# Performance work log

Measured on AMD Instinct MI355X. Metric: run time of the kernel, lower is better.

The kernel has to match this reference:

```python
import jax, jax.numpy as jnp
import numpy as np
from jax import lax

HMA = 8.0
H = W = 34
A = 15
IMH = IMW = 270.0
AW = jnp.array([9.232984,16.0,27.712813,18.465969,32.0,55.425626,36.931937,64.0,110.851252,73.863875,128.0,221.702503,147.72775,256.0,443.405007], jnp.float32)
AH = jnp.array([27.72668,16.0,9.237604,55.453359,32.0,18.475209,110.906719,64.0,36.950417,221.813438,128.0,73.900834,443.626876,256.0,147.801669], jnp.float32)
RPN_MEAN = jnp.array([0.000437,0.002586,-0.123953,-0.081469], jnp.float32)
RPN_STD = jnp.array([0.12677,0.095741,0.3173,0.281042], jnp.float32)
RCNN_STD = jnp.array([0.1,0.1,0.2,0.2], jnp.float32)
RPN_MIN = 6.16056
RCNN_MIN = 8.8008
NUM_CLASS = 3

def _decode(t, acx, acy, aw, ah):
    cx = t[..., 0] * aw + acx
    cy = t[..., 1] * ah + acy
    bw = jnp.exp(t[..., 2]) * aw
    bh = jnp.exp(t[..., 3]) * ah
    x1 = jnp.clip(cx - 0.5 * (bw - 1.0), 0.0, IMW - 1.0)
    y1 = jnp.clip(cy - 0.5 * (bh - 1.0), 0.0, IMH - 1.0)
    x2 = jnp.clip(cx + 0.5 * (bw - 1.0), 0.0, IMW - 1.0)
    y2 = jnp.clip(cy + 0.5 * (bh - 1.0), 0.0, IMH - 1.0)
    return jnp.stack([x1, y1, x2, y2], -1)

def _nms(boxes, scores, thresh, top_n):
    # greedy hard NMS, fixed top_n output with validity mask
    x1, y1, x2, y2 = boxes[:, 0], boxes[:, 1], boxes[:, 2], boxes[:, 3]
    areas = (x2 - x1 + 1.0) * (y2 - y1 + 1.0)
    n = boxes.shape[0]
    def step(scur, _):
        j = jnp.argmax(scur)
        valid = scur[j] > 0.0
        bj = boxes[j]
        iw = jnp.maximum(jnp.minimum(x2, bj[2]) - jnp.maximum(x1, bj[0]) + 1.0, 0.0)
        ih = jnp.maximum(jnp.minimum(y2, bj[3]) - jnp.maximum(y1, bj[1]) + 1.0, 0.0)
        inter = iw * ih
        iou = inter / (areas + areas[j] - inter)
        sup = (iou > thresh) | (jnp.arange(n) == j)
        return jnp.where(sup, -1.0, scur), (j, valid)
    _, (idx, valid) = lax.scan(step, scores, None, length=top_n)
    return idx, valid

def _psroi_one(ftr, roi):
    # ftr: [10,7,7,H,W] position-sensitive features; roi: [x1,y1,x2,y2] image coords
    sw = roi[0] / HMA; sh = roi[1] / HMA
    ew = (roi[2] + 1.0) / HMA; eh = (roi[3] + 1.0) / HMA
    rh = jnp.maximum(eh - sh, 0.1); rw = jnp.maximum(ew - sw, 0.1)
    bh = rh / 7.0; bw = rw / 7.0
    g = jnp.arange(7, dtype=jnp.float32); s = jnp.arange(4, dtype=jnp.float32)
    ys = sh + g[:, None] * bh + (s[None, :] + 0.5) * (bh / 4.0)  # [7(ph),4]
    xs = sw + g[:, None] * bw + (s[None, :] + 0.5) * (bw / 4.0)  # [7(pw),4]
    y0 = jnp.floor(ys); x0 = jnp.floor(xs)
    dy = ys - y0; dx = xs - x0
    y0i = y0.astype(jnp.int32); x0i = x0.astype(jnp.int32)
    c = jnp.arange(10)[:, None, None, None, None]
    P = jnp.arange(7)[None, :, None, None, None]
    Q = jnp.arange(7)[None, None, :, None, None]
    def corner(yi, xi, wy, wx):
        my = ((yi >= 0) & (yi < H)).astype(jnp.float32)
        mx = ((xi >= 0) & (xi < W)).astype(jnp.float32)
        yc = jnp.clip(yi, 0, H - 1); xc = jnp.clip(xi, 0, W - 1)
        v = ftr[c, P, Q, yc[None, :, None, :, None], xc[None, None, :, None, :]]
        return v * (wy * my)[None, :, None, :, None] * (wx * mx)[None, None, :, None, :]
    val = (corner(y0i, x0i, 1 - dy, 1 - dx) + corner(y0i, x0i + 1, 1 - dy, dx)
         + corner(y0i + 1, x0i, dy, 1 - dx) + corner(y0i + 1, x0i + 1, dy, dx))
    return val.mean(axis=(3, 4))  # [10,7,7]

def reference(rpn_cls_prob_reshape, rpn_bbox_pred, ft_add_left_right, W_inner, b_inner, W_cls, b_cls, W_bbox, b_bbox):
    # ---------- RPNProposalSSD ----------
    fg = rpn_cls_prob_reshape[0, A:, :, :].reshape(-1)  # [A*H*W] fg probs
    t = rpn_bbox_pred[0].reshape(A, 4, H, W).transpose(0, 2, 3, 1)  # [A,H,W,4]
    t = t * RPN_STD + RPN_MEAN
    acx = (jnp.arange(W, dtype=jnp.float32) * HMA)[None, None, :]
    acy = (jnp.arange(H, dtype=jnp.float32) * HMA)[None, :, None]
    boxes = _decode(t, acx, acy, AW[:, None, None], AH[:, None, None]).reshape(-1, 4)
    bw = boxes[:, 2] - boxes[:, 0] + 1.0; bh = boxes[:, 3] - boxes[:, 1] + 1.0
    keep = (fg >= 0.2) & ((bw >= RPN_MIN) | (bh >= RPN_MIN))
    top_s, top_i = lax.top_k(jnp.where(keep, fg, -1.0), 3000)
    cand = boxes[top_i]
    idx, valid = _nms(cand, top_s, 0.7, 300)
    vm = valid.astype(jnp.float32)[:, None]
    rois_xy = cand[idx] * vm  # [300,4], padded rows zeroed
    rois = jnp.concatenate([jnp.zeros((300, 1), jnp.float32), rois_xy], axis=1)
    rpn_scores = top_s[idx][:, None] * vm  # [300,1]
    # ---------- DFMBPSROIAlign ----------
    ftr = ft_add_left_right[0].reshape(10, 7, 7, H, W)
    pooled = jax.vmap(lambda r: _psroi_one(ftr, r))(rois_xy)  # [300,10,7,7]
    # ---------- FC head ----------
    feat = jax.nn.relu(pooled.reshape(-1, 490) @ W_inner.T + b_inner)
    probs = jax.nn.softmax(feat @ W_cls.T + b_cls, axis=1)  # [300,4]
    bpred = feat @ W_bbox.T + b_bbox  # [300,16]
    # ---------- RCNNProposal ----------
    rw = rois_xy[:, 2] - rois_xy[:, 0] + 1.0; rh2 = rois_xy[:, 3] - rois_xy[:, 1] + 1.0
    rcx = rois_xy[:, 0] + 0.5 * (rw - 1.0); rcy = rois_xy[:, 1] + 0.5 * (rh2 - 1.0)
    obj_ok = (1.0 - probs[:, 0]) >= 0.1
    all_b, all_s, all_l, all_k = [], [], [], []
    for cidx in range(1, NUM_CLASS + 1):
        tc = bpred[:, 4 * cidx:4 * cidx + 4] * RCNN_STD  # rcnn mean is 0
        db = _decode(tc, rcx, rcy, rw, rh2)
        dw = db[:, 2] - db[:, 0] + 1.0; dh = db[:, 3] - db[:, 1] + 1.0
        sc = probs[:, cidx]
        k = valid & obj_ok & (sc >= 0.1) & ((dw >= RCNN_MIN) | (dh >= RCNN_MIN))
        all_b.append(db); all_s.append(sc)
        all_l.append(jnp.full((300,), float(cidx), jnp.float32)); all_k.append(k)
    cb = jnp.concatenate(all_b); cs = jnp.concatenate(all_s)
    cl = jnp.concatenate(all_l); ck = jnp.concatenate(all_k)
    ts2, ti2 = lax.top_k(jnp.where(ck, cs, -1.0), 300)
    cand2 = cb[ti2]; lab2 = cl[ti2]
    idx2, val2 = _nms(cand2, ts2, 0.5, 5)
    v2 = val2.astype(jnp.float32)
    bboxes = jnp.concatenate([cand2[idx2] * v2[:, None], (ts2[idx2] * v2)[:, None], (lab2[idx2] * v2)[:, None]], axis=1)  # [5,6] x1,y1,x2,y2,score,label
    return bboxes, rois, rpn_scores

def setup_inputs() -> dict:
    key = jax.random.key(0)
    ks = jax.random.split(key, 6)
    return {
        'rpn_cls_prob_reshape': jax.random.uniform(ks[0], (1, 2 * A, H, W), jnp.float32),
        'rpn_bbox_pred': jax.random.normal(ks[1], (1, 4 * A, H, W), jnp.float32) * 0.5,
        'ft_add_left_right': jax.random.normal(ks[2], (1, 490, H, W), jnp.float32),
        'W_inner': jax.random.normal(ks[3], (2048, 490), jnp.float32) * 0.02,
        'b_inner': jnp.zeros((2048,), jnp.float32),
        'W_cls': jax.random.normal(ks[4], (4, 2048), jnp.float32) * 0.02,
        'b_cls': jnp.zeros((4,), jnp.float32),
        'W_bbox': jax.random.normal(ks[5], (16, 2048), jnp.float32) * 0.02,
        'b_bbox': jnp.zeros((16,), jnp.float32),
    }
```

## Files before the change

kernel.cpp:

```cpp
#include <hip/hip_runtime.h>

#define NB 17340
#define TOPK1 3000
#define TOPK2 300
#define PTS 304

__constant__ float c_AW[15] = {9.232984, 16.0, 27.712813, 18.465969, 32.0, 55.425626,
                               36.931937, 64.0, 110.851252, 73.863875, 128.0, 221.702503,
                               147.72775, 256.0, 443.405007};
__constant__ float c_AH[15] = {27.72668, 16.0, 9.237604, 55.453359, 32.0, 18.475209,
                               110.906719, 64.0, 36.950417, 221.813438, 128.0, 73.900834,
                               443.626876, 256.0, 147.801669};

__device__ __forceinline__ unsigned mapf(float f) {
  unsigned u = __float_as_uint(f);
  return (u & 0x80000000u) ? ~u : (u | 0x80000000u);
}
__device__ __forceinline__ float unmapf(unsigned m) {
  unsigned u = (m & 0x80000000u) ? (m & 0x7FFFFFFFu) : ~m;
  return __uint_as_float(u);
}
__device__ __forceinline__ float clipc(float v) {
  return fminf(fmaxf(v, 0.0f), 269.0f);
}
__device__ __forceinline__ unsigned long long readlane64(unsigned long long v, int lane) {
  unsigned lo = (unsigned)__builtin_amdgcn_readlane((int)(unsigned)v, lane);
  unsigned hi = (unsigned)__builtin_amdgcn_readlane((int)(unsigned)(v >> 32), lane);
  return ((unsigned long long)hi << 32) | lo;
}

__global__ void k_decode(const float* __restrict__ cls, const float* __restrict__ pred,
                         float* __restrict__ boxes, float* __restrict__ scores,
                         unsigned int* __restrict__ hist) {
  int i = blockIdx.x * 256 + threadIdx.x;
  if (i >= NB) return;
  int a = i / 1156;
  int rem = i - a * 1156;
  int y = rem / 34;
  int x = rem - y * 34;
  float fg = cls[(15 + a) * 1156 + rem];
  const float* p = pred + a * 4 * 1156 + rem;
  float t0 = p[0]    * (float)0.12677  + (float)0.000437;
  float t1 = p[1156] * (float)0.095741 + (float)0.002586;
  float t2 = p[2312] * (float)0.3173   + (float)-0.123953;
  float t3 = p[3468] * (float)0.281042 + (float)-0.081469;
  float aw = c_AW[a], ah = c_AH[a];
  float cx = t0 * aw + (float)x * 8.0f;
  float cy = t1 * ah + (float)y * 8.0f;
  float bw = expf(t2) * aw;
  float bh = expf(t3) * ah;
  float x1 = clipc(cx - 0.5f * (bw - 1.0f));
  float y1 = clipc(cy - 0.5f * (bh - 1.0f));
  float x2 = clipc(cx + 0.5f * (bw - 1.0f));
  float y2 = clipc(cy + 0.5f * (bh - 1.0f));
  boxes[i * 4 + 0] = x1;
  boxes[i * 4 + 1] = y1;
  boxes[i * 4 + 2] = x2;
  boxes[i * 4 + 3] = y2;
  float w2 = x2 - x1 + 1.0f, h2 = y2 - y1 + 1.0f;
  bool keep = (fg >= 0.2f) && ((w2 >= (float)6.16056) || (h2 >= (float)6.16056));
  scores[i] = keep ? fg : -1.0f;
  if (keep) atomicAdd(&hist[mapf(fg) >> 18], 1u);
}

__global__ __launch_bounds__(256) void k_cutoff(const unsigned int* __restrict__ hist,
                                                unsigned int* __restrict__ bcut) {
  const int t = threadIdx.x;
  __shared__ unsigned int sh[16384];
  __shared__ unsigned int coarse[256];
  for (int i = t; i < 16384; i += 256) sh[i] = hist[i];
  __syncthreads();
  {
    unsigned s = 0;
    int b0 = t * 64;
    for (int b = 0; b < 64; ++b) s += sh[b0 + b];
    coarse[t] = s;
  }
  __syncthreads();
  if (t == 0) {
    unsigned acc = 0, nbefore = 0;
    int C = 0;
    for (int c = 255; c >= 0; --c) {
      if (acc + coarse[c] >= (unsigned)TOPK1) { C = c; nbefore = acc; break; }
      acc += coarse[c];
    }
    unsigned acc2 = nbefore;
    int B = C * 64;
    for (int b = C * 64 + 63; b >= C * 64; --b) {
      if (acc2 + sh[b] >= (unsigned)TOPK1) { B = b; break; }
      acc2 += sh[b];
    }
    bcut[0] = (unsigned)B;
  }
}

__global__ __launch_bounds__(256) void k_compact(const float* __restrict__ scores,
                                                 const unsigned int* __restrict__ bcut,
                                                 unsigned int* __restrict__ cnt,
                                                 unsigned long long* __restrict__ keys) {
  int i = blockIdx.x * 256 + threadIdx.x;
  const unsigned B = bcut[0];
  if (i < NB) {
    unsigned m = mapf(scores[i]);
    if ((m >> 18) >= B) {
      unsigned p = atomicAdd(cnt, 1u);
      if (p < 4096u) keys[p] = ((unsigned long long)m << 15) | (unsigned)(32767 - i);
    }
  }
}

__global__ __launch_bounds__(256) void k_sort(const float* __restrict__ boxes,
                                              const unsigned int* __restrict__ cnt,
                                              const unsigned long long* __restrict__ keys,
                                              unsigned int* __restrict__ sscore,
                                              float4* __restrict__ sbox) {
  const int t = threadIdx.x;
  __shared__ unsigned long long lk[4096];
  const int K = min((int)cnt[0], 4096);
  for (int i = t; i < 4096; i += 256) lk[i] = (i < K) ? keys[i] : 0ull;
  __syncthreads();
  int p = blockIdx.x * 32 + (t >> 3);
  const int s = t & 7;
  if (p < K) {
    unsigned long long kp = lk[p];
    int r = 0;
    for (int q = s; q < 4096; q += 64) {
#pragma unroll
      for (int u = 0; u < 8; ++u) r += (lk[q + 8 * u] > kp) ? 1 : 0;
    }
    r += __shfl_xor(r, 1);
    r += __shfl_xor(r, 2);
    r += __shfl_xor(r, 4);
    if (s == 0 && r < TOPK1) {
      int idx = 32767 - (int)(kp & 32767ull);
      sscore[r] = (unsigned)(kp >> 15);
      sbox[r] = ((const float4*)boxes)[idx];
    }
  }
}

__global__ __launch_bounds__(64) void k_iou(const float4* __restrict__ sbox,
                                            unsigned long long* __restrict__ mat) {
  const int wi = blockIdx.x, wj = blockIdx.y;
  if (wj < wi) return;
  __shared__ float4 cb[64];
  __shared__ float car[64];
  const int l = threadIdx.x;
  float4 c = sbox[wj * 64 + l];
  cb[l] = c;
  car[l] = (c.z - c.x + 1.0f) * (c.w - c.y + 1.0f);
  __syncthreads();
  const int ri = wi * 64 + l;
  float4 r = sbox[ri];
  float rar = (r.z - r.x + 1.0f) * (r.w - r.y + 1.0f);
  unsigned long long m = 0ull;
#pragma unroll 16
  for (int j = 0; j < 64; ++j) {
    float4 cc = cb[j];
    float iw = fmaxf(fminf(r.z, cc.z) - fmaxf(r.x, cc.x) + 1.0f, 0.0f);
    float ih = fmaxf(fminf(r.w, cc.w) - fmaxf(r.y, cc.y) + 1.0f, 0.0f);
    float inter = iw * ih;
    float iou = inter / (car[j] + rar - inter);
    if (iou > 0.7f) m |= (1ull << j);
  }
  mat[ri * 48 + wj] = m;
}

__global__ __launch_bounds__(256) void k_nms1(const unsigned int* __restrict__ sscore,
                                              const float4* __restrict__ sbox,
                                              const unsigned long long* __restrict__ mat,
                                              float* __restrict__ dout,
                                              float* __restrict__ rois_xy,
                                              float* __restrict__ validf) {
  const int t = threadIdx.x;
  __shared__ unsigned long long rowbuf[2][64][48];
  __shared__ unsigned int sc[3008];
  __shared__ int arank[300];
  __shared__ int s_A;
  for (int i = t; i < 3008; i += 256) sc[i] = (i < TOPK1) ? sscore[i] : 0u;
  if (t == 0) s_A = 0;

  {
    unsigned long long r0v[12];
#pragma unroll
    for (int i = 0; i < 12; ++i) r0v[i] = mat[t + 256 * i];
#pragma unroll
    for (int i = 0; i < 12; ++i) {
      int idx = t + 256 * i;
      rowbuf[0][idx / 48][idx % 48] = r0v[i];
    }
  }
  unsigned long long rgA[16], rgB[16];
  const int st = t - 64;
  if (t >= 64) {
#pragma unroll
    for (int i = 0; i < 16; ++i) rgA[i] = mat[1 * 3072 + st + 192 * i];
#pragma unroll
    for (int i = 0; i < 16; ++i) rgB[i] = mat[2 * 3072 + st + 192 * i];
  }
  __syncthreads();

  unsigned long long run = 0ull;
  int A = 0;
  const int l = t & 63;
  const int lw = (l < 48) ? l : 0;
  for (int c = 0; c < 47; ++c) {
    if (t < 64) {
      const bool okw = (l >= c) && (l < 47);
      unsigned long long supw = readlane64(run, c);
      bool aliveb = (sc[c * 64 + l] > 0x80000000u) && !((supw >> l) & 1ull);
      unsigned long long alive = __ballot(aliveb);
      int Aw = A;
      const int buf = c & 1;
      while (alive != 0ull && Aw < 300) {
        int j1 = __ffsll((long long)alive) - 1;
        unsigned long long rest = alive & (alive - 1ull);
        int j2 = (rest != 0ull) ? (__ffsll((long long)rest) - 1) : -1;
        unsigned long long v1 = rowbuf[buf][j1][lw];
        unsigned long long v2 = rowbuf[buf][(j2 >= 0 ? j2 : j1)][lw];
        if (l == 0) arank[Aw] = c * 64 + j1;
        Aw++;
        unsigned long long kill1 = readlane64(v1, c);
        run |= okw ? v1 : 0ull;
        alive &= ~kill1;
        if (j2 >= 0 && ((alive >> j2) & 1ull) && Aw < 300) {
          if (l == 0) arank[Aw] = c * 64 + j2;
          Aw++;
          unsigned long long kill2 = readlane64(v2, c);
          run |= okw ? v2 : 0ull;
          alive &= ~kill2;
        }
      }
      A = Aw;
      if (l == 0) s_A = Aw;
    } else if (c < 46) {
      int nb = (c + 1) & 1;
      if (((c + 1) & 1) == 1) {
#pragma unroll
        for (int i = 0; i < 16; ++i) {
          int idx = st + 192 * i;
          rowbuf[nb][idx / 48][idx % 48] = rgA[i];
        }
        if (c + 3 <= 46) {
#pragma unroll
          for (int i = 0; i < 16; ++i) rgA[i] = mat[(c + 3) * 3072 + st + 192 * i];
        }
      } else {
#pragma unroll
        for (int i = 0; i < 16; ++i) {
          int idx = st + 192 * i;
          rowbuf[nb][idx / 48][idx % 48] = rgB[i];
        }
        if (c + 3 <= 46) {
#pragma unroll
          for (int i = 0; i < 16; ++i) rgB[i] = mat[(c + 3) * 3072 + st + 192 * i];
        }
      }
    }
    __syncthreads();
    A = s_A;
    if (A >= 300) break;
    if (c < 46 && sc[(c + 1) * 64] <= 0x80000000u) break;
  }
  for (int a = t; a < A; a += 256) {
    int rk = arank[a];
    float4 b = sbox[rk];
    dout[30 + a * 5 + 0] = 0.0f;
    dout[30 + a * 5 + 1] = b.x;
    dout[30 + a * 5 + 2] = b.y;
    dout[30 + a * 5 + 3] = b.z;
    dout[30 + a * 5 + 4] = b.w;
    dout[1530 + a] = unmapf(sc[rk]);
    rois_xy[a * 4 + 0] = b.x; rois_xy[a * 4 + 1] = b.y;
    rois_xy[a * 4 + 2] = b.z; rois_xy[a * 4 + 3] = b.w;
    validf[a] = 1.0f;
  }
  for (int z = 30 + A * 5 + t; z < 1530; z += 256) dout[z] = 0.f;
  for (int z = 1530 + A + t; z < 1830; z += 256) dout[z] = 0.f;
  for (int z = A * 4 + t; z < 1200; z += 256) rois_xy[z] = 0.f;
  for (int z = A + t; z < 300; z += 256) validf[z] = 0.f;
}

__global__ __launch_bounds__(256) void k_psroi(const float* __restrict__ ft,
                                               const float* __restrict__ rois_xy,
                                               float* __restrict__ pooledT) {
  int r = blockIdx.x;
  __shared__ int2 ycs[28];
  __shared__ float2 wys[28];
  __shared__ int2 xcs[28];
  __shared__ float2 wxs[28];
  float r0 = rois_xy[r * 4 + 0], r1 = rois_xy[r * 4 + 1];
  float r2 = rois_xy[r * 4 + 2], r3 = rois_xy[r * 4 + 3];
  float sw = r0 * 0.125f;
  float sh = r1 * 0.125f;
  float ew = (r2 + 1.0f) * 0.125f;
  float eh = (r3 + 1.0f) * 0.125f;
  float rh = fmaxf(eh - sh, 0.1f);
  float rw = fmaxf(ew - sw, 0.1f);
  float bh = rh / 7.0f;
  float bwd = rw / 7.0f;
  const int t = threadIdx.x;
  if (t < 28) {
    int p = t >> 2, sy = t & 3;
    float ys = sh + (float)p * bh + ((float)sy + 0.5f) * (bh * 0.25f);
    float y0f = floorf(ys);
    float dy = ys - y0f;
    int y0 = (int)y0f;
    float wy0 = (1.0f - dy) * ((y0 >= 0 && y0 < 34) ? 1.f : 0.f);
    float wy1 = dy * ((y0 + 1 >= 0 && y0 + 1 < 34) ? 1.f : 0.f);
    ycs[t] = make_int2(min(max(y0, 0), 33), min(max(y0 + 1, 0), 33));
    wys[t] = make_float2(wy0, wy1);
  } else if (t >= 32 && t < 60) {
    int q = (t - 32) >> 2, sx = (t - 32) & 3;
    float xs = sw + (float)q * bwd + ((float)sx + 0.5f) * (bwd * 0.25f);
    float x0f = floorf(xs);
    float dx = xs - x0f;
    int x0 = (int)x0f;
    float wx0 = (1.0f - dx) * ((x0 >= 0 && x0 < 34) ? 1.f : 0.f);
    float wx1 = dx * ((x0 + 1 >= 0 && x0 + 1 < 34) ? 1.f : 0.f);
    xcs[t - 32] = make_int2(min(max(x0, 0), 33), min(max(x0 + 1, 0), 33));
    wxs[t - 32] = make_float2(wx0, wx1);
  }
  __syncthreads();
  for (int o = t; o < 490; o += 256) {
    int pq = o % 49;
    int p = pq / 7, q = pq - p * 7;
    const float* base = ft + o * 1156;
    float acc = 0.f;
#pragma unroll
    for (int sy = 0; sy < 4; ++sy) {
      int2 yc = ycs[p * 4 + sy];
      float2 wy = wys[p * 4 + sy];
#pragma unroll
      for (int sx = 0; sx < 4; ++sx) {
        int2 xc = xcs[q * 4 + sx];
        float2 wx = wxs[q * 4 + sx];
        float v00 = base[yc.x * 34 + xc.x], v01 = base[yc.x * 34 + xc.y];
        float v10 = base[yc.y * 34 + xc.x], v11 = base[yc.y * 34 + xc.y];
        acc += wy.x * wx.x * v00 + wy.x * wx.y * v01 + wy.y * wx.x * v10 + wy.y * wx.y * v11;
      }
    }
    pooledT[o * PTS + r] = acc * (1.0f / 16.0f);
  }
}

__global__ __launch_bounds__(256) void k_fc1(const float* __restrict__ pooledT,
                                             const float* __restrict__ Wi,
                                             const float* __restrict__ bi,
                                             float* __restrict__ feat) {
  __shared__ float As[2][32][68];
  __shared__ float Bs[2][32][36];
  const int t = threadIdx.x;
  const int tr = t >> 4, tc = t & 15;
  const int b = blockIdx.x;
  const int xcd = b & 7, s = b >> 3;
  const int r0 = (s % 5) * 64;
  const int o0 = (xcd + 8 * (s / 5)) * 32;
  float acc[4][2];
#pragma unroll
  for (int i = 0; i < 4; ++i) { acc[i][0] = 0.f; acc[i][1] = 0.f; }
  float ra[8], rb[4];

#pragma unroll
  for (int i = 0; i < 8; ++i) {
    int idx = t + 256 * i;
    int kk = idx >> 6, rr = idx & 63;
    ra[i] = (kk < 490 && r0 + rr < 300) ? pooledT[kk * PTS + r0 + rr] : 0.f;
  }
#pragma unroll
  for (int i = 0; i < 4; ++i) {
    int idx = t + 256 * i;
    int oo = idx >> 5, k2 = idx & 31;
    rb[i] = Wi[(o0 + oo) * 490 + k2];
  }
#pragma unroll
  for (int i = 0; i < 8; ++i) {
    int idx = t + 256 * i;
    As[0][idx >> 6][idx & 63] = ra[i];
  }
#pragma unroll
  for (int i = 0; i < 4; ++i) {
    int idx = t + 256 * i;
    Bs[0][idx & 31][idx >> 5] = rb[i];
  }
  __syncthreads();

  int cur = 0;
  for (int step = 0; step < 16; ++step) {
    if (step < 15) {
      int k0n = (step + 1) * 32;
#pragma unroll
      for (int i = 0; i < 8; ++i) {
        int idx = t + 256 * i;
        int kk = idx >> 6, rr = idx & 63;
        int k = k0n + kk;
        ra[i] = (k < 490 && r0 + rr < 300) ? pooledT[k * PTS + r0 + rr] : 0.f;
      }
#pragma unroll
      for (int i = 0; i < 4; ++i) {
        int idx = t + 256 * i;
        int oo = idx >> 5, k2 = k0n + (idx & 31);
        rb[i] = (k2 < 490) ? Wi[(o0 + oo) * 490 + k2] : 0.f;
      }
    }
#pragma unroll
    for (int kk = 0; kk < 32; ++kk) {
      float4 a4 = *(const float4*)&As[cur][kk][tr * 4];
      float2 b2 = *(const float2*)&Bs[cur][kk][tc * 2];
      acc[0][0] += a4.x * b2.x; acc[0][1] += a4.x * b2.y;
      acc[1][0] += a4.y * b2.x; acc[1][1] += a4.y * b2.y;
      acc[2][0] += a4.z * b2.x; acc[2][1] += a4.z * b2.y;
      acc[3][0] += a4.w * b2.x; acc[3][1] += a4.w * b2.y;
    }
    if (step < 15) {
      int nxt = cur ^ 1;
#pragma unroll
      for (int i = 0; i < 8; ++i) {
        int idx = t + 256 * i;
        As[nxt][idx >> 6][idx & 63] = ra[i];
      }
#pragma unroll
      for (int i = 0; i < 4; ++i) {
        int idx = t + 256 * i;
        Bs[nxt][idx & 31][idx >> 5] = rb[i];
      }
      cur = nxt;
    }
    __syncthreads();
  }
  float2 bias = *(const float2*)&bi[o0 + tc * 2];
#pragma unroll
  for (int i = 0; i < 4; ++i) {
    int r = r0 + tr * 4 + i;
    if (r < 300) {
      float2 v;
      v.x = fmaxf(acc[i][0] + bias.x, 0.f);
      v.y = fmaxf(acc[i][1] + bias.y, 0.f);
      *(float2*)&feat[r * 2048 + o0 + tc * 2] = v;
    }
  }
}

__global__ __launch_bounds__(256) void k_fc2(const float* __restrict__ feat,
                                             const float* __restrict__ Wc,
                                             const float* __restrict__ bc,
                                             const float* __restrict__ Wb,
                                             const float* __restrict__ bb,
                                             const float* __restrict__ rois_xy,
                                             const float* __restrict__ validf,
                                             float* __restrict__ db2,
                                             float* __restrict__ msc2) {
  int r = blockIdx.x;
  int t = threadIdx.x;
  int l = t & 63, w = t >> 6;
  __shared__ float frow[2048];
  __shared__ float s_logit[20];
  __shared__ float s_probs[4];
  for (int i = t; i < 512; i += 256)
    ((float4*)frow)[i] = ((const float4*)(feat + r * 2048))[i];
  __syncthreads();
  for (int o = w; o < 20; o += 4) {
    const float* wr = (o < 4) ? (Wc + o * 2048) : (Wb + (o - 4) * 2048);
    float p = 0.f;
#pragma unroll
    for (int j = 0; j < 8; ++j) {
      float4 wv = ((const float4*)wr)[l + 64 * j];
      float4 fv = ((const float4*)frow)[l + 64 * j];
      p += wv.x * fv.x + wv.y * fv.y + wv.z * fv.z + wv.w * fv.w;
    }
    for (int off = 32; off > 0; off >>= 1) p += __shfl_xor(p, off);
    if (l == 0) s_logit[o] = p + ((o < 4) ? bc[o] : bb[o - 4]);
  }
  __syncthreads();
  if (t == 0) {
    float m = fmaxf(fmaxf(s_logit[0], s_logit[1]), fmaxf(s_logit[2], s_logit[3]));
    float e0 = expf(s_logit[0] - m), e1 = expf(s_logit[1] - m);
    float e2 = expf(s_logit[2] - m), e3 = expf(s_logit[3] - m);
    float ssum = e0 + e1 + e2 + e3;
    s_probs[0] = e0 / ssum; s_probs[1] = e1 / ssum;
    s_probs[2] = e2 / ssum; s_probs[3] = e3 / ssum;
  }
  __syncthreads();
  if (t < 3) {
    int c = t + 1;
    float x1 = rois_xy[r * 4 + 0], y1 = rois_xy[r * 4 + 1];
    float x2 = rois_xy[r * 4 + 2], y2 = rois_xy[r * 4 + 3];
    float rwv = x2 - x1 + 1.0f, rhv = y2 - y1 + 1.0f;
    float rcx = x1 + 0.5f * (rwv - 1.0f), rcy = y1 + 0.5f * (rhv - 1.0f);
    float t0 = s_logit[4 + 4 * c + 0] * 0.1f;
    float t1 = s_logit[4 + 4 * c + 1] * 0.1f;
    float t2 = s_logit[4 + 4 * c + 2] * 0.2f;
    float t3 = s_logit[4 + 4 * c + 3] * 0.2f;
    float cx = t0 * rwv + rcx, cy = t1 * rhv + rcy;
    float bw = expf(t2) * rwv, bh = expf(t3) * rhv;
    float dx1 = clipc(cx - 0.5f * (bw - 1.0f));
    float dy1 = clipc(cy - 0.5f * (bh - 1.0f));
    float dx2 = clipc(cx + 0.5f * (bw - 1.0f));
    float dy2 = clipc(cy + 0.5f * (bh - 1.0f));
    float dw = dx2 - dx1 + 1.0f, dh = dy2 - dy1 + 1.0f;
    float sc = s_probs[c];
    bool objok = (1.0f - s_probs[0]) >= 0.1f;
    bool valid = validf[r] > 0.5f;
    bool kf = valid && objok && (sc >= 0.1f) && ((dw >= (float)8.8008) || (dh >= (float)8.8008));
    int i2 = (c - 1) * 300 + r;
    db2[i2 * 4 + 0] = dx1; db2[i2 * 4 + 1] = dy1;
    db2[i2 * 4 + 2] = dx2; db2[i2 * 4 + 3] = dy2;
    msc2[i2] = kf ? sc : -1.0f;
  }
}

__global__ __launch_bounds__(1024) void k_nms2(const float* __restrict__ db2,
                                               const float* __restrict__ msc2,
                                               float* __restrict__ dout) {
  const int t = threadIdx.x;
  __shared__ unsigned long long lk[1024];
  __shared__ unsigned long long sk[1024];
  __shared__ float4 abox[5];
  __shared__ float aar[5];
  __shared__ int s_A;
  sk[t] = 0ull;
  lk[t] = (t < 900) ? (((unsigned long long)mapf(msc2[t]) << 10) | (unsigned)(1023 - t)) : 0ull;
  if (t == 0) s_A = 0;
  __syncthreads();
  if (t < 900) {
    unsigned long long kp = lk[t];
    int r = 0;
#pragma unroll 8
    for (int q = 0; q < 1024; ++q) r += (lk[q] > kp) ? 1 : 0;
    sk[r] = kp;
  }
  __syncthreads();
  if (t < 64) {
    int A = 0;
    for (int base = 0; base < TOPK2 && A < 5; base += 64) {
      unsigned headm = (unsigned)(sk[base] >> 10);
      if (headm <= 0x80000000u) break;
      int rank = base + t;
      unsigned long long key = sk[rank];
      unsigned mk = (unsigned)(key >> 10);
      bool active = (rank < TOPK2) && (mk > 0x80000000u);
      int idx = 1023 - (int)(key & 1023ull);
      float4 bx = make_float4(0.f, 0.f, 0.f, 0.f);
      float area = 0.f;
      if (active) {
        bx = ((const float4*)db2)[idx];
        area = (bx.z - bx.x + 1.0f) * (bx.w - bx.y + 1.0f);
      }
      bool alive = active;
      for (int a = 0; a < A; ++a) {
        float4 ab = abox[a];
        float iw = fmaxf(fminf(bx.z, ab.z) - fmaxf(bx.x, ab.x) + 1.0f, 0.0f);
        float ih = fmaxf(fminf(bx.w, ab.w) - fmaxf(bx.y, ab.y) + 1.0f, 0.0f);
        float inter = iw * ih;
        float iou = inter / (area + aar[a] - inter);
        if (iou > 0.5f) { alive = false; break; }
      }
      unsigned long long bal = __ballot(alive);
      while (bal != 0ull && A < 5) {
        int j = __ffsll((long long)bal) - 1;
        float jx1 = __shfl(bx.x, j), jy1 = __shfl(bx.y, j);
        float jx2 = __shfl(bx.z, j), jy2 = __shfl(bx.w, j);
        float jar = __shfl(area, j);
        if (t == j) {
          abox[A] = bx; aar[A] = area;
          dout[A * 6 + 0] = bx.x; dout[A * 6 + 1] = bx.y;
          dout[A * 6 + 2] = bx.z; dout[A * 6 + 3] = bx.w;
          dout[A * 6 + 4] = unmapf(mk);
          dout[A * 6 + 5] = (float)(idx / 300 + 1);
        }
        if (alive) {
          float iw = fmaxf(fminf(bx.z, jx2) - fmaxf(bx.x, jx1) + 1.0f, 0.0f);
          float ih = fmaxf(fminf(bx.w, jy2) - fmaxf(bx.y, jy1) + 1.0f, 0.0f);
          float inter = iw * ih;
          float iou = inter / (area + jar - inter);
          if (iou > 0.5f || t == j) alive = false;
        }
        A++;
        bal = __ballot(alive);
      }
    }
    if (t == 0) s_A = A;
  }
  __syncthreads();
  int A = s_A;
  for (int z = A * 6 + t; z < 30; z += 1024) dout[z] = 0.f;
}

extern "C" void kernel_launch(void* const* d_in, const int* in_sizes, int n_in,
                              void* d_out, int out_size, void* d_ws, size_t ws_size,
                              hipStream_t stream) {
  const float* cls  = (const float*)d_in[0];
  const float* pred = (const float*)d_in[1];
  const float* ft   = (const float*)d_in[2];
  const float* Wi   = (const float*)d_in[3];
  const float* bi   = (const float*)d_in[4];
  const float* Wc   = (const float*)d_in[5];
  const float* bc   = (const float*)d_in[6];
  const float* Wb   = (const float*)d_in[7];
  const float* bb   = (const float*)d_in[8];
  float* out = (float*)d_out;
  float* w = (float*)d_ws;
  float* boxes   = w;
  float* scores  = w + 69360;
  unsigned int* hist = (unsigned int*)(w + 86700);
  unsigned int* cnt  = (unsigned int*)(w + 103084);
  unsigned int* bcut = (unsigned int*)(w + 103085);
  unsigned long long* keys = (unsigned long long*)(w + 103088);
  unsigned int* sscore = (unsigned int*)(w + 111280);
  float4* sbox   = (float4*)(w + 114280);
  float* rois_xy = w + 126312;
  float* validf  = w + 127512;
  float* pooledT = w + 127812;
  float* feat    = w + 276772;
  unsigned long long* mat = (unsigned long long*)(w + 276772);
  float* db2     = w + 891172;
  float* msc2    = w + 894772;

  hipMemsetAsync(hist, 0, 16385 * sizeof(unsigned int), stream);
  k_decode<<<68, 256, 0, stream>>>(cls, pred, boxes, scores, hist);
  k_cutoff<<<1, 256, 0, stream>>>(hist, bcut);
  k_compact<<<68, 256, 0, stream>>>(scores, bcut, cnt, keys);
  k_sort<<<128, 256, 0, stream>>>(boxes, cnt, keys, sscore, sbox);
  k_iou<<<dim3(47, 47), 64, 0, stream>>>(sbox, mat);
  k_nms1<<<1, 256, 0, stream>>>(sscore, sbox, mat, out, rois_xy, validf);
  k_psroi<<<300, 256, 0, stream>>>(ft, rois_xy, pooledT);
  k_fc1<<<320, 256, 0, stream>>>(pooledT, Wi, bi, feat);
  k_fc2<<<300, 256, 0, stream>>>(feat, Wc, bc, Wb, bb, rois_xy, validf, db2, msc2);
  k_nms2<<<1, 1024, 0, stream>>>(db2, msc2, out);
}
```

Baseline: 195.4 us.

## Fuse proposal front-end stages into one cooperative persistent kernel

Merges the histogram memset, decode, cutoff, compaction, rank sort, IoU bitmask and first NMS into one cooperative kernel of 128 blocks. Grid-wide syncs separate the stages, replacing six kernel launches and a memset. The goal is to remove per-launch overhead and inter-kernel gaps across these small stages. In exchange it pays for five grid barriers, and the IoU tiles now run as a grid-stride loop over 4 waves per block instead of one block per tile.

```diff
diff --git a/kernel.cpp b/kernel.cpp
--- a/kernel.cpp
+++ b/kernel.cpp
@@ -1,4 +1,6 @@
 #include <hip/hip_runtime.h>
+#include <hip/hip_cooperative_groups.h>
+namespace cg = cooperative_groups;
 
 #define NB 17340
 #define TOPK1 3000
@@ -29,256 +31,280 @@
   return ((unsigned long long)hi << 32) | lo;
 }
 
-__global__ void k_decode(const float* __restrict__ cls, const float* __restrict__ pred,
-                         float* __restrict__ boxes, float* __restrict__ scores,
-                         unsigned int* __restrict__ hist) {
-  int i = blockIdx.x * 256 + threadIdx.x;
-  if (i >= NB) return;
-  int a = i / 1156;
-  int rem = i - a * 1156;
-  int y = rem / 34;
-  int x = rem - y * 34;
-  float fg = cls[(15 + a) * 1156 + rem];
-  const float* p = pred + a * 4 * 1156 + rem;
-  float t0 = p[0]    * (float)0.12677  + (float)0.000437;
-  float t1 = p[1156] * (float)0.095741 + (float)0.002586;
-  float t2 = p[2312] * (float)0.3173   + (float)-0.123953;
-  float t3 = p[3468] * (float)0.281042 + (float)-0.081469;
-  float aw = c_AW[a], ah = c_AH[a];
-  float cx = t0 * aw + (float)x * 8.0f;
-  float cy = t1 * ah + (float)y * 8.0f;
-  float bw = expf(t2) * aw;
-  float bh = expf(t3) * ah;
-  float x1 = clipc(cx - 0.5f * (bw - 1.0f));
-  float y1 = clipc(cy - 0.5f * (bh - 1.0f));
-  float x2 = clipc(cx + 0.5f * (bw - 1.0f));
-  float y2 = clipc(cy + 0.5f * (bh - 1.0f));
-  boxes[i * 4 + 0] = x1;
-  boxes[i * 4 + 1] = y1;
-  boxes[i * 4 + 2] = x2;
-  boxes[i * 4 + 3] = y2;
-  float w2 = x2 - x1 + 1.0f, h2 = y2 - y1 + 1.0f;
-  bool keep = (fg >= 0.2f) && ((w2 >= (float)6.16056) || (h2 >= (float)6.16056));
-  scores[i] = keep ? fg : -1.0f;
-  if (keep) atomicAdd(&hist[mapf(fg) >> 18], 1u);
-}
-
-__global__ __launch_bounds__(256) void k_cutoff(const unsigned int* __restrict__ hist,
-                                                unsigned int* __restrict__ bcut) {
+__global__ __launch_bounds__(256) void k_front(const float* __restrict__ cls,
+                                               const float* __restrict__ pred,
+                                               float* __restrict__ boxes,
+                                               float* __restrict__ scores,
+                                               unsigned int* __restrict__ hist,
+                                               unsigned int* __restrict__ bcut,
+                                               unsigned int* __restrict__ cnt,
+                                               unsigned long long* __restrict__ keys,
+                                               unsigned int* __restrict__ sscore,
+                                               float4* __restrict__ sbox,
+                                               unsigned long long* __restrict__ mat,
+                                               float* __restrict__ dout,
+                                               float* __restrict__ rois_xy,
+                                               float* __restrict__ validf) {
+  cg::grid_group grid = cg::this_grid();
+  __shared__ __align__(16) unsigned char smem[66560];
   const int t = threadIdx.x;
-  __shared__ unsigned int sh[16384];
-  __shared__ unsigned int coarse[256];
-  for (int i = t; i < 16384; i += 256) sh[i] = hist[i];
-  __syncthreads();
+  const int b = blockIdx.x;
+  const int gid = b * 256 + t;
+  const int gstride = gridDim.x * 256;
+
+  for (int i = gid; i < 16385; i += gstride) hist[i] = 0u;
+  __threadfence();
+  grid.sync();
+
+  for (int i = gid; i < NB; i += gstride) {
+    int a = i / 1156;
+    int rem = i - a * 1156;
+    int y = rem / 34;
+    int x = rem - y * 34;
+    float fg = cls[(15 + a) * 1156 + rem];
+    const float* p = pred + a * 4 * 1156 + rem;
+    float t0 = p[0]    * (float)0.12677  + (float)0.000437;
+    float t1 = p[1156] * (float)0.095741 + (float)0.002586;
+    float t2 = p[2312] * (float)0.3173   + (float)-0.123953;
+    float t3 = p[3468] * (float)0.281042 + (float)-0.081469;
+    float aw = c_AW[a], ah = c_AH[a];
+    float cx = t0 * aw + (float)x * 8.0f;
+    float cy = t1 * ah + (float)y * 8.0f;
+    float bw = expf(t2) * aw;
+    float bh = expf(t3) * ah;
+    float x1 = clipc(cx - 0.5f * (bw - 1.0f));
+    float y1 = clipc(cy - 0.5f * (bh - 1.0f));
+    float x2 = clipc(cx + 0.5f * (bw - 1.0f));
+    float y2 = clipc(cy + 0.5f * (bh - 1.0f));
+    boxes[i * 4 + 0] = x1;
+    boxes[i * 4 + 1] = y1;
+    boxes[i * 4 + 2] = x2;
+    boxes[i * 4 + 3] = y2;
+    float w2 = x2 - x1 + 1.0f, h2 = y2 - y1 + 1.0f;
+    bool keep = (fg >= 0.2f) && ((w2 >= (float)6.16056) || (h2 >= (float)6.16056));
+    scores[i] = keep ? fg : -1.0f;
+    if (keep) atomicAdd(&hist[mapf(fg) >> 18], 1u);
+  }
+  __threadfence();
+  grid.sync();
+
+  if (b == 0) {
+    unsigned int* sh = (unsigned int*)smem;
+    unsigned int* coarse = (unsigned int*)(smem + 65536);
+    for (int i = t; i < 16384; i += 256) sh[i] = hist[i];
+    __syncthreads();
+    {
+      unsigned s = 0;
+      int b0 = t * 64;
+      for (int k = 0; k < 64; ++k) s += sh[b0 + k];
+      coarse[t] = s;
+    }
+    __syncthreads();
+    if (t == 0) {
+      unsigned acc = 0, nbefore = 0;
+      int C = 0;
+      for (int c = 255; c >= 0; --c) {
+        if (acc + coarse[c] >= (unsigned)TOPK1) { C = c; nbefore = acc; break; }
+        acc += coarse[c];
+      }
+      unsigned acc2 = nbefore;
+      int B = C * 64;
+      for (int k = C * 64 + 63; k >= C * 64; --k) {
+        if (acc2 + sh[k] >= (unsigned)TOPK1) { B = k; break; }
+        acc2 += sh[k];
+      }
+      bcut[0] = (unsigned)B;
+    }
+  }
+  __threadfence();
+  grid.sync();
+
   {
-    unsigned s = 0;
-    int b0 = t * 64;
-    for (int b = 0; b < 64; ++b) s += sh[b0 + b];
-    coarse[t] = s;
-  }
-  __syncthreads();
-  if (t == 0) {
-    unsigned acc = 0, nbefore = 0;
-    int C = 0;
-    for (int c = 255; c >= 0; --c) {
-      if (acc + coarse[c] >= (unsigned)TOPK1) { C = c; nbefore = acc; break; }
-      acc += coarse[c];
-    }
-    unsigned acc2 = nbefore;
-    int B = C * 64;
-    for (int b = C * 64 + 63; b >= C * 64; --b) {
-      if (acc2 + sh[b] >= (unsigned)TOPK1) { B = b; break; }
-      acc2 += sh[b];
-    }
-    bcut[0] = (unsigned)B;
-  }
-}
-
-__global__ __launch_bounds__(256) void k_compact(const float* __restrict__ scores,
-                                                 const unsigned int* __restrict__ bcut,
-                                                 unsigned int* __restrict__ cnt,
-                                                 unsigned long long* __restrict__ keys) {
-  int i = blockIdx.x * 256 + threadIdx.x;
-  const unsigned B = bcut[0];
-  if (i < NB) {
-    unsigned m = mapf(scores[i]);
-    if ((m >> 18) >= B) {
-      unsigned p = atomicAdd(cnt, 1u);
-      if (p < 4096u) keys[p] = ((unsigned long long)m << 15) | (unsigned)(32767 - i);
-    }
-  }
-}
-
-__global__ __launch_bounds__(256) void k_sort(const float* __restrict__ boxes,
-                                              const unsigned int* __restrict__ cnt,
-                                              const unsigned long long* __restrict__ keys,
-                                              unsigned int* __restrict__ sscore,
-                                              float4* __restrict__ sbox) {
-  const int t = threadIdx.x;
-  __shared__ unsigned long long lk[4096];
-  const int K = min((int)cnt[0], 4096);
-  for (int i = t; i < 4096; i += 256) lk[i] = (i < K) ? keys[i] : 0ull;
-  __syncthreads();
-  int p = blockIdx.x * 32 + (t >> 3);
-  const int s = t & 7;
-  if (p < K) {
-    unsigned long long kp = lk[p];
-    int r = 0;
-    for (int q = s; q < 4096; q += 64) {
-#pragma unroll
-      for (int u = 0; u < 8; ++u) r += (lk[q + 8 * u] > kp) ? 1 : 0;
-    }
-    r += __shfl_xor(r, 1);
-    r += __shfl_xor(r, 2);
-    r += __shfl_xor(r, 4);
-    if (s == 0 && r < TOPK1) {
-      int idx = 32767 - (int)(kp & 32767ull);
-      sscore[r] = (unsigned)(kp >> 15);
-      sbox[r] = ((const float4*)boxes)[idx];
-    }
-  }
-}
-
-__global__ __launch_bounds__(64) void k_iou(const float4* __restrict__ sbox,
-                                            unsigned long long* __restrict__ mat) {
-  const int wi = blockIdx.x, wj = blockIdx.y;
-  if (wj < wi) return;
-  __shared__ float4 cb[64];
-  __shared__ float car[64];
-  const int l = threadIdx.x;
-  float4 c = sbox[wj * 64 + l];
-  cb[l] = c;
-  car[l] = (c.z - c.x + 1.0f) * (c.w - c.y + 1.0f);
-  __syncthreads();
-  const int ri = wi * 64 + l;
-  float4 r = sbox[ri];
-  float rar = (r.z - r.x + 1.0f) * (r.w - r.y + 1.0f);
-  unsigned long long m = 0ull;
+    const unsigned B = bcut[0];
+    for (int i = gid; i < NB; i += gstride) {
+      unsigned m = mapf(scores[i]);
+      if ((m >> 18) >= B) {
+        unsigned p = atomicAdd(cnt, 1u);
+        if (p < 4096u) keys[p] = ((unsigned long long)m << 15) | (unsigned)(32767 - i);
+      }
+    }
+  }
+  __threadfence();
+  grid.sync();
+
+  {
+    unsigned long long* lk = (unsigned long long*)smem;
+    const int K = min((int)cnt[0], 4096);
+    for (int i = t; i < 4096; i += 256) lk[i] = (i < K) ? keys[i] : 0ull;
+    __syncthreads();
+    int p = b * 32 + (t >> 3);
+    const int s = t & 7;
+    if (p < K) {
+      unsigned long long kp = lk[p];
+      int r = 0;
+      for (int q = s; q < 4096; q += 64) {
+#pragma unroll
+        for (int u = 0; u < 8; ++u) r += (lk[q + 8 * u] > kp) ? 1 : 0;
+      }
+      r += __shfl_xor(r, 1);
+      r += __shfl_xor(r, 2);
+      r += __shfl_xor(r, 4);
+      if (s == 0 && r < TOPK1) {
+        int idx = 32767 - (int)(kp & 32767ull);
+        sscore[r] = (unsigned)(kp >> 15);
+        sbox[r] = ((const float4*)boxes)[idx];
+      }
+    }
+    __syncthreads();
+  }
+  __threadfence();
+  grid.sync();
+
+  {
+    float4* cb = (float4*)smem;
+    float* car = (float*)(smem + 4096);
+    const int wv = t >> 6, l = t & 63;
+    for (int base = b * 4; base < 2209; base += 512) {
+      int tile = base + wv;
+      int wi = tile / 47, wj = tile - wi * 47;
+      bool act = (tile < 2209) && (wj >= wi);
+      __syncthreads();
+      if (act) {
+        float4 c = sbox[wj * 64 + l];
+        cb[wv * 64 + l] = c;
+        car[wv * 64 + l] = (c.z - c.x + 1.0f) * (c.w - c.y + 1.0f);
+      }
+      __syncthreads();
+      if (act) {
+        int ri = wi * 64 + l;
+        float4 r = sbox[ri];
+        float rar = (r.z - r.x + 1.0f) * (r.w - r.y + 1.0f);
+        unsigned long long m = 0ull;
 #pragma unroll 16
-  for (int j = 0; j < 64; ++j) {
-    float4 cc = cb[j];
-    float iw = fmaxf(fminf(r.z, cc.z) - fmaxf(r.x, cc.x) + 1.0f, 0.0f);
-    float ih = fmaxf(fminf(r.w, cc.w) - fmaxf(r.y, cc.y) + 1.0f, 0.0f);
-    float inter = iw * ih;
-    float iou = inter / (car[j] + rar - inter);
-    if (iou > 0.7f) m |= (1ull << j);
-  }
-  mat[ri * 48 + wj] = m;
-}
-
-__global__ __launch_bounds__(256) void k_nms1(const unsigned int* __restrict__ sscore,
-                                              const float4* __restrict__ sbox,
-                                              const unsigned long long* __restrict__ mat,
-                                              float* __restrict__ dout,
-                                              float* __restrict__ rois_xy,
-                                              float* __restrict__ validf) {
-  const int t = threadIdx.x;
-  __shared__ unsigned long long rowbuf[2][64][48];
-  __shared__ unsigned int sc[3008];
-  __shared__ int arank[300];
-  __shared__ int s_A;
-  for (int i = t; i < 3008; i += 256) sc[i] = (i < TOPK1) ? sscore[i] : 0u;
-  if (t == 0) s_A = 0;
-
+        for (int j = 0; j < 64; ++j) {
+          float4 cc = cb[wv * 64 + j];
+          float iw = fmaxf(fminf(r.z, cc.z) - fmaxf(r.x, cc.x) + 1.0f, 0.0f);
+          float ih = fmaxf(fminf(r.w, cc.w) - fmaxf(r.y, cc.y) + 1.0f, 0.0f);
+          float inter = iw * ih;
+          float iou = inter / (car[wv * 64 + j] + rar - inter);
+          if (iou > 0.7f) m |= (1ull << j);
+        }
+        mat[ri * 48 + wj] = m;
+      }
+    }
+  }
+  __threadfence();
+  grid.sync();
+
+  if (b != 0) return;
   {
-    unsigned long long r0v[12];
-#pragma unroll
-    for (int i = 0; i < 12; ++i) r0v[i] = mat[t + 256 * i];
-#pragma unroll
-    for (int i = 0; i < 12; ++i) {
-      int idx = t + 256 * i;
-      rowbuf[0][idx / 48][idx % 48] = r0v[i];
-    }
-  }
-  unsigned long long rgA[16], rgB[16];
-  const int st = t - 64;
-  if (t >= 64) {
-#pragma unroll
-    for (int i = 0; i < 16; ++i) rgA[i] = mat[1 * 3072 + st + 192 * i];
-#pragma unroll
-    for (int i = 0; i < 16; ++i) rgB[i] = mat[2 * 3072 + st + 192 * i];
-  }
-  __syncthreads();
-
-  unsigned long long run = 0ull;
-  int A = 0;
-  const int l = t & 63;
-  const int lw = (l < 48) ? l : 0;
-  for (int c = 0; c < 47; ++c) {
-    if (t < 64) {
-      const bool okw = (l >= c) && (l < 47);
-      unsigned long long supw = readlane64(run, c);
-      bool aliveb = (sc[c * 64 + l] > 0x80000000u) && !((supw >> l) & 1ull);
-      unsigned long long alive = __ballot(aliveb);
-      int Aw = A;
-      const int buf = c & 1;
-      while (alive != 0ull && Aw < 300) {
-        int j1 = __ffsll((long long)alive) - 1;
-        unsigned long long rest = alive & (alive - 1ull);
-        int j2 = (rest != 0ull) ? (__ffsll((long long)rest) - 1) : -1;
-        unsigned long long v1 = rowbuf[buf][j1][lw];
-        unsigned long long v2 = rowbuf[buf][(j2 >= 0 ? j2 : j1)][lw];
-        if (l == 0) arank[Aw] = c * 64 + j1;
-        Aw++;
-        unsigned long long kill1 = readlane64(v1, c);
-        run |= okw ? v1 : 0ull;
-        alive &= ~kill1;
-        if (j2 >= 0 && ((alive >> j2) & 1ull) && Aw < 300) {
-          if (l == 0) arank[Aw] = c * 64 + j2;
+    unsigned long long (*rowbuf)[64][48] = (unsigned long long (*)[64][48])smem;
+    unsigned int* sc = (unsigned int*)(smem + 49152);
+    int* arank = (int*)(smem + 61184);
+    int* s_A = (int*)(smem + 62384);
+    for (int i = t; i < 3008; i += 256) sc[i] = (i < TOPK1) ? sscore[i] : 0u;
+    if (t == 0) s_A[0] = 0;
+
+    {
+      unsigned long long r0v[12];
+#pragma unroll
+      for (int i = 0; i < 12; ++i) r0v[i] = mat[t + 256 * i];
+#pragma unroll
+      for (int i = 0; i < 12; ++i) {
+        int idx = t + 256 * i;
+        rowbuf[0][idx / 48][idx % 48] = r0v[i];
+      }
+    }
+    unsigned long long rgA[16], rgB[16];
+    const int st = t - 64;
+    if (t >= 64) {
+#pragma unroll
+      for (int i = 0; i < 16; ++i) rgA[i] = mat[1 * 3072 + st + 192 * i];
+#pragma unroll
+      for (int i = 0; i < 16; ++i) rgB[i] = mat[2 * 3072 + st + 192 * i];
+    }
+    __syncthreads();
+
+    unsigned long long run = 0ull;
+    int A = 0;
+    const int l = t & 63;
+    const int lw = (l < 48) ? l : 0;
+    for (int c = 0; c < 47; ++c) {
+      if (t < 64) {
+        const bool okw = (l >= c) && (l < 47);
+        unsigned long long supw = readlane64(run, c);
+        bool aliveb = (sc[c * 64 + l] > 0x80000000u) && !((supw >> l) & 1ull);
+        unsigned long long alive = __ballot(aliveb);
+        int Aw = A;
+        const int buf = c & 1;
+        while (alive != 0ull && Aw < 300) {
+          int j1 = __ffsll((long long)alive) - 1;
+          unsigned long long rest = alive & (alive - 1ull);
+          int j2 = (rest != 0ull) ? (__ffsll((long long)rest) - 1) : -1;
+          unsigned long long v1 = rowbuf[buf][j1][lw];
+          unsigned long long v2 = rowbuf[buf][(j2 >= 0 ? j2 : j1)][lw];
+          if (l == 0) arank[Aw] = c * 64 + j1;
           Aw++;
-          unsigned long long kill2 = readlane64(v2, c);
-          run |= okw ? v2 : 0ull;
-          alive &= ~kill2;
+          unsigned long long kill1 = readlane64(v1, c);
+          run |= okw ? v1 : 0ull;
+          alive &= ~kill1;
+          if (j2 >= 0 && ((alive >> j2) & 1ull) && Aw < 300) {
+            if (l == 0) arank[Aw] = c * 64 + j2;
+            Aw++;
+            unsigned long long kill2 = readlane64(v2, c);
+            run |= okw ? v2 : 0ull;
+            alive &= ~kill2;
+          }
         }
-      }
-      A = Aw;
-      if (l == 0) s_A = Aw;
-    } else if (c < 46) {
-      int nb = (c + 1) & 1;
-      if (((c + 1) & 1) == 1) {
-#pragma unroll
-        for (int i = 0; i < 16; ++i) {
-          int idx = st + 192 * i;
-          rowbuf[nb][idx / 48][idx % 48] = rgA[i];
+        A = Aw;
+        if (l == 0) s_A[0] = Aw;
+      } else if (c < 46) {
+        int nb = (c + 1) & 1;
+        if (((c + 1) & 1) == 1) {
+#pragma unroll
+          for (int i = 0; i < 16; ++i) {
+            int idx = st + 192 * i;
+            rowbuf[nb][idx / 48][idx % 48] = rgA[i];
+          }
+          if (c + 3 <= 46) {
+#pragma unroll
+            for (int i = 0; i < 16; ++i) rgA[i] = mat[(c + 3) * 3072 + st + 192 * i];
+          }
+        } else {
+#pragma unroll
+          for (int i = 0; i < 16; ++i) {
+            int idx = st + 192 * i;
+            rowbuf[nb][idx / 48][idx % 48] = rgB[i];
+          }
+          if (c + 3 <= 46) {
+#pragma unroll
+            for (int i = 0; i < 16; ++i) rgB[i] = mat[(c + 3) * 3072 + st + 192 * i];
+          }
         }
-        if (c + 3 <= 46) {
-#pragma unroll
-          for (int i = 0; i < 16; ++i) rgA[i] = mat[(c + 3) * 3072 + st + 192 * i];
-        }
-      } else {
-#pragma unroll
-        for (int i = 0; i < 16; ++i) {
-          int idx = st + 192 * i;
-          rowbuf[nb][idx / 48][idx % 48] = rgB[i];
-        }
-        if (c + 3 <= 46) {
-#pragma unroll
-          for (int i = 0; i < 16; ++i) rgB[i] = mat[(c + 3) * 3072 + st + 192 * i];
-        }
-      }
-    }
-    __syncthreads();
-    A = s_A;
-    if (A >= 300) break;
-    if (c < 46 && sc[(c + 1) * 64] <= 0x80000000u) break;
-  }
-  for (int a = t; a < A; a += 256) {
-    int rk = arank[a];
-    float4 b = sbox[rk];
-    dout[30 + a * 5 + 0] = 0.0f;
-    dout[30 + a * 5 + 1] = b.x;
-    dout[30 + a * 5 + 2] = b.y;
-    dout[30 + a * 5 + 3] = b.z;
-    dout[30 + a * 5 + 4] = b.w;
-    dout[1530 + a] = unmapf(sc[rk]);
-    rois_xy[a * 4 + 0] = b.x; rois_xy[a * 4 + 1] = b.y;
-    rois_xy[a * 4 + 2] = b.z; rois_xy[a * 4 + 3] = b.w;
-    validf[a] = 1.0f;
-  }
-  for (int z = 30 + A * 5 + t; z < 1530; z += 256) dout[z] = 0.f;
-  for (int z = 1530 + A + t; z < 1830; z += 256) dout[z] = 0.f;
-  for (int z = A * 4 + t; z < 1200; z += 256) rois_xy[z] = 0.f;
-  for (int z = A + t; z < 300; z += 256) validf[z] = 0.f;
+      }
+      __syncthreads();
+      A = s_A[0];
+      if (A >= 300) break;
+      if (c < 46 && sc[(c + 1) * 64] <= 0x80000000u) break;
+    }
+    for (int a = t; a < A; a += 256) {
+      int rk = arank[a];
+      float4 bx = sbox[rk];
+      dout[30 + a * 5 + 0] = 0.0f;
+      dout[30 + a * 5 + 1] = bx.x;
+      dout[30 + a * 5 + 2] = bx.y;
+      dout[30 + a * 5 + 3] = bx.z;
+      dout[30 + a * 5 + 4] = bx.w;
+      dout[1530 + a] = unmapf(sc[rk]);
+      rois_xy[a * 4 + 0] = bx.x; rois_xy[a * 4 + 1] = bx.y;
+      rois_xy[a * 4 + 2] = bx.z; rois_xy[a * 4 + 3] = bx.w;
+      validf[a] = 1.0f;
+    }
+    for (int z = 30 + A * 5 + t; z < 1530; z += 256) dout[z] = 0.f;
+    for (int z = 1530 + A + t; z < 1830; z += 256) dout[z] = 0.f;
+    for (int z = A * 4 + t; z < 1200; z += 256) rois_xy[z] = 0.f;
+    for (int z = A + t; z < 300; z += 256) validf[z] = 0.f;
+  }
 }
 
 __global__ __launch_bounds__(256) void k_psroi(const float* __restrict__ ft,
@@ -616,13 +642,11 @@
   float* db2     = w + 891172;
   float* msc2    = w + 894772;
 
-  hipMemsetAsync(hist, 0, 16385 * sizeof(unsigned int), stream);
-  k_decode<<<68, 256, 0, stream>>>(cls, pred, boxes, scores, hist);
-  k_cutoff<<<1, 256, 0, stream>>>(hist, bcut);
-  k_compact<<<68, 256, 0, stream>>>(scores, bcut, cnt, keys);
-  k_sort<<<128, 256, 0, stream>>>(boxes, cnt, keys, sscore, sbox);
-  k_iou<<<dim3(47, 47), 64, 0, stream>>>(sbox, mat);
-  k_nms1<<<1, 256, 0, stream>>>(sscore, sbox, mat, out, rois_xy, validf);
+  void* kargs[] = { (void*)&cls, (void*)&pred, (void*)&boxes, (void*)&scores,
+                    (void*)&hist, (void*)&bcut, (void*)&cnt, (void*)&keys,
+                    (void*)&sscore, (void*)&sbox, (void*)&mat, (void*)&out,
+                    (void*)&rois_xy, (void*)&validf };
+  hipLaunchCooperativeKernel((const void*)k_front, dim3(128), dim3(256), kargs, 0, stream);
   k_psroi<<<300, 256, 0, stream>>>(ft, rois_xy, pooledT);
   k_fc1<<<320, 256, 0, stream>>>(pooledT, Wi, bi, feat);
   k_fc2<<<300, 256, 0, stream>>>(feat, Wc, bc, Wb, bb, rois_xy, validf, db2, msc2);
```

Result: slower. 331.3 us (+69.6%).
